# Performance work log

Hardware: AMD Instinct MI355X
Metric: run time of the kernel (lower is better)

The kernel has to match this reference:

```python
import jax, jax.numpy as jnp
import numpy as np

NUM_NODES, MEM_DIM, MSG_DIM, TIME_DIM = 65536, 128, 128, 128
POS_DIM = MEM_DIM  # PositionMessage reshape forces pos_embedding_dim == memory_dim
IN_MEM = MSG_DIM + 2 * MEM_DIM + TIME_DIM  # IdentityMessage width = 512
IN_POS = POS_DIM + 2 * MEM_DIM + TIME_DIM  # PositionMessage width = 512


def setup_inputs() -> dict:
    key = jax.random.key(0)
    ks = jax.random.split(key, 24)
    s = jnp.float32(0.05)
    f = lambda k, sh: jax.random.normal(k, sh, jnp.float32)
    return dict(
        n_id=jnp.arange(NUM_NODES, dtype=jnp.int32),
        memory=f(ks[0], (NUM_NODES, MEM_DIM)),
        pos_mem=f(ks[1], (NUM_NODES, MEM_DIM)),
        pos_emb=f(ks[2], (NUM_NODES, POS_DIM)),
        raw_msg_s=f(ks[3], (NUM_NODES, MSG_DIM)),
        raw_msg_d=f(ks[4], (NUM_NODES, MSG_DIM)),
        other_s=jax.random.randint(ks[5], (NUM_NODES,), 0, NUM_NODES, jnp.int32),
        other_d=jax.random.randint(ks[6], (NUM_NODES,), 0, NUM_NODES, jnp.int32),
        t_s=jax.random.randint(ks[7], (NUM_NODES,), 1000, 2000, jnp.int32),
        t_d=jax.random.randint(ks[8], (NUM_NODES,), 1000, 2000, jnp.int32),
        last_update=jax.random.randint(ks[9], (NUM_NODES,), 0, 1000, jnp.int32),
        w_time_mem=f(ks[10], (TIME_DIM,)) * s, b_time_mem=f(ks[11], (TIME_DIM,)) * s,
        w_time_pos=f(ks[12], (TIME_DIM,)) * s, b_time_pos=f(ks[13], (TIME_DIM,)) * s,
        Wih_mem=f(ks[14], (3 * MEM_DIM, IN_MEM)) * s, Whh_mem=f(ks[15], (3 * MEM_DIM, MEM_DIM)) * s,
        bih_mem=f(ks[16], (3 * MEM_DIM,)) * s, bhh_mem=f(ks[17], (3 * MEM_DIM,)) * s,
        Wih_pos=f(ks[18], (3 * MEM_DIM, IN_POS)) * s, Whh_pos=f(ks[19], (3 * MEM_DIM, MEM_DIM)) * s,
        bih_pos=f(ks[20], (3 * MEM_DIM,)) * s, bhh_pos=f(ks[21], (3 * MEM_DIM,)) * s,
    )


def _time_enc(t_rel, w, b):
    # PyG TimeEncoder: cos(Linear(1, time_dim)(t_rel))
    return jnp.cos(t_rel[:, None] * w[None, :] + b[None, :])


def _gru(x, h, Wih, Whh, bih, bhh):
    # torch.nn.GRUCell math
    gi = x @ Wih.T + bih
    gh = h @ Whh.T + bhh
    ir, iz, inn = jnp.split(gi, 3, axis=-1)
    hr, hz, hn = jnp.split(gh, 3, axis=-1)
    r = jax.nn.sigmoid(ir + hr)
    z = jax.nn.sigmoid(iz + hz)
    n = jnp.tanh(inn + r * hn)
    return (1.0 - z) * n + z * h


def _tgn_memory(mem, n_id, other_s, other_d, feat_s, feat_d, t_s, t_d,
                last_update, w_t, b_t, Wih, Whh, bih, bhh):
    # Gather per-node state; each node owns one src-store and one dst-store message.
    h = mem[n_id]                                        # [N, D]
    lu = last_update[n_id].astype(jnp.float32)
    te_s = _time_enc(t_s.astype(jnp.float32) - lu, w_t, b_t)
    te_d = _time_enc(t_d.astype(jnp.float32) - lu, w_t, b_t)
    msg_s = jnp.concatenate([h, mem[other_s], feat_s, te_s], axis=-1)  # [N, IN]
    msg_d = jnp.concatenate([h, mem[other_d], feat_d, te_d], axis=-1)
    # LastAggregator: keep the most recent message per node (scatter_max on t)
    pick_s = (t_s >= t_d)[:, None]
    aggr = jnp.where(pick_s, msg_s, msg_d)
    z = _gru(aggr, h, Wih, Whh, bih, bhh)
    new_lu = jnp.maximum(t_s, t_d)
    return z, new_lu


def reference(n_id, memory, pos_mem, pos_emb, raw_msg_s, raw_msg_d,
              other_s, other_d, t_s, t_d, last_update,
              w_time_mem, b_time_mem, w_time_pos, b_time_pos,
              Wih_mem, Whh_mem, bih_mem, bhh_mem,
              Wih_pos, Whh_pos, bih_pos, bhh_pos):
    z, last_up = _tgn_memory(memory, n_id, other_s, other_d, raw_msg_s, raw_msg_d,
                             t_s, t_d, last_update,
                             w_time_mem, b_time_mem, Wih_mem, Whh_mem, bih_mem, bhh_mem)
    # pos raw message is the event's src node id -> embedding lookup
    pos_z, _ = _tgn_memory(pos_mem, n_id, other_s, other_d,
                           pos_emb[n_id], pos_emb[other_d],
                           t_s, t_d, last_update,
                           w_time_pos, b_time_pos, Wih_pos, Whh_pos, bih_pos, bhh_pos)
    return z, pos_z, last_up
```

## Files before the change

kernel.cpp:

```cpp
#include <hip/hip_runtime.h>
#include <hip/hip_bf16.h>
#include <math.h>

#define NODES   65536
#define DD      128
#define BM      64
#define NSUB    24
#define WTILE_STRIDE (NSUB * 64 * 8)
#define WG_STRIDE    (20 * WTILE_STRIDE)

typedef __bf16 bf16x8 __attribute__((ext_vector_type(8)));
typedef float  f32x4  __attribute__((ext_vector_type(4)));

static __device__ __forceinline__ unsigned short f2bf(float f) {
    union { float f; unsigned u; } v; v.f = f;
    return (unsigned short)((v.u + 0x8000u) >> 16);
}
static __device__ __forceinline__ ushort4 pack4(float4 v) {
    ushort4 p;
    p.x = f2bf(v.x); p.y = f2bf(v.y); p.z = f2bf(v.z); p.w = f2bf(v.w);
    return p;
}
static __device__ __forceinline__ float fastcos(float x) {
    float r = x * 0.15915494309189535f;
    r = r - floorf(r);
    return __builtin_amdgcn_cosf(r);
}
static __device__ __forceinline__ float fsigmoid(float x) {
    return 1.0f / (1.0f + __expf(-x));
}
static __device__ __forceinline__ float ftanh(float x) {
    float ax = fabsf(x);
    float t  = __expf(-2.0f * ax);
    float th = 1.0f - 2.0f * t / (1.0f + t);
    return copysignf(th, x);
}

__global__ void prep_w_kernel(const float* __restrict__ Wih0, const float* __restrict__ Whh0,
                              const float* __restrict__ Wih1, const float* __restrict__ Whh1,
                              unsigned short* __restrict__ Wws) {
    int gid = blockIdx.x * 256 + threadIdx.x;
    if (gid >= 2 * WG_STRIDE) return;
    int g   = gid / WG_STRIDE;
    int r   = gid - g * WG_STRIDE;
    int kt  = r / WTILE_STRIDE;
    int r2  = r - kt * WTILE_STRIDE;
    int t   = r2 >> 9;
    int l8  = r2 & 511;
    int lane = l8 >> 3, j = l8 & 7;
    int cl  = lane & 15, q = lane >> 4;
    int n   = t * 16 + cl;
    const float* Wih = g ? Wih1 : Wih0;
    const float* Whh = g ? Whh1 : Whh0;
    float v;
    if (kt < 16) v = Wih[n * 512 + kt * 32 + q * 8 + j];
    else         v = Whh[n * 128 + (kt - 16) * 32 + q * 8 + j];
    Wws[gid] = f2bf(v);
}


#define KTILE(st)                                                              \
    do {                                                                       \
        bf16x8 a[4];                                                           \
        _Pragma("unroll")                                                      \
        for (int j = 0; j < 4; ++j)                                            \
            a[j] = *(const bf16x8*)(Xb + (j * 16 + cl) * 1024 +                \
                                    (((st) * 64 + q * 16) ^ swz));             \
        const unsigned short* wk = wbase + (size_t)(st) * WTILE_STRIDE;        \
        bf16x8 bR = *(const bf16x8*)(wk + tR * 512);                           \
        bf16x8 bZ = *(const bf16x8*)(wk + tZ * 512);                           \
        bf16x8 bN = *(const bf16x8*)(wk + tN * 512);                           \
        _Pragma("unroll")                                                      \
        for (int j = 0; j < 4; ++j) {                                          \
            acc[j * 4 + 0] = __builtin_amdgcn_mfma_f32_16x16x32_bf16(a[j], bR, acc[j * 4 + 0], 0, 0, 0); \
            acc[j * 4 + 1] = __builtin_amdgcn_mfma_f32_16x16x32_bf16(a[j], bZ, acc[j * 4 + 1], 0, 0, 0); \
            acc[j * 4 + 2] = __builtin_amdgcn_mfma_f32_16x16x32_bf16(a[j], bN, acc[j * 4 + 2], 0, 0, 0); \
        }                                                                      \
    } while (0)

#define KTILE2(st)                                                             \
    do {                                                                       \
        bf16x8 a[4];                                                           \
        _Pragma("unroll")                                                      \
        for (int j = 0; j < 4; ++j)                                            \
            a[j] = *(const bf16x8*)(Xb + (j * 16 + cl) * 1024 +                \
                                    (((st) * 64 + q * 16) ^ swz));             \
        const unsigned short* wk = wbase + (size_t)(st) * WTILE_STRIDE;        \
        const unsigned short* wh = wbase + (size_t)(16 + (st)) * WTILE_STRIDE; \
        bf16x8 bR = *(const bf16x8*)(wk + tR * 512);                           \
        bf16x8 bZ = *(const bf16x8*)(wk + tZ * 512);                           \
        bf16x8 bN = *(const bf16x8*)(wk + tN * 512);                           \
        bf16x8 cR = *(const bf16x8*)(wh + tR * 512);                           \
        bf16x8 cZ = *(const bf16x8*)(wh + tZ * 512);                           \
        bf16x8 cN = *(const bf16x8*)(wh + tN * 512);                           \
        _Pragma("unroll")                                                      \
        for (int j = 0; j < 4; ++j) {                                          \
            acc[j * 4 + 0] = __builtin_amdgcn_mfma_f32_16x16x32_bf16(a[j], bR, acc[j * 4 + 0], 0, 0, 0); \
            acc[j * 4 + 1] = __builtin_amdgcn_mfma_f32_16x16x32_bf16(a[j], bZ, acc[j * 4 + 1], 0, 0, 0); \
            acc[j * 4 + 2] = __builtin_amdgcn_mfma_f32_16x16x32_bf16(a[j], bN, acc[j * 4 + 2], 0, 0, 0); \
            acc[j * 4 + 0] = __builtin_amdgcn_mfma_f32_16x16x32_bf16(a[j], cR, acc[j * 4 + 0], 0, 0, 0); \
            acc[j * 4 + 1] = __builtin_amdgcn_mfma_f32_16x16x32_bf16(a[j], cZ, acc[j * 4 + 1], 0, 0, 0); \
            acc[j * 4 + 3] = __builtin_amdgcn_mfma_f32_16x16x32_bf16(a[j], cN, acc[j * 4 + 3], 0, 0, 0); \
        }                                                                      \
    } while (0)

__global__ __launch_bounds__(512, 4) void tgn_fused_kernel(
    const int*   __restrict__ n_id,
    const float* __restrict__ memory_,
    const float* __restrict__ pos_mem,
    const float* __restrict__ pos_emb,
    const float* __restrict__ raw_s,
    const float* __restrict__ raw_d,
    const int*   __restrict__ other_s,
    const int*   __restrict__ other_d,
    const int*   __restrict__ t_s,
    const int*   __restrict__ t_d,
    const int*   __restrict__ last_update,
    const float* __restrict__ w_time_mem, const float* __restrict__ b_time_mem,
    const float* __restrict__ w_time_pos, const float* __restrict__ b_time_pos,
    const float* __restrict__ bih_mem, const float* __restrict__ bhh_mem,
    const float* __restrict__ bih_pos, const float* __restrict__ bhh_pos,
    const unsigned short* __restrict__ Wws,
    float* __restrict__ out)
{
    __shared__ __align__(16) unsigned short X[BM * 512];
    __shared__ int   snid[BM];
    __shared__ int   soth[BM];
    __shared__ float sdt[BM];
    __shared__ int   sfeat[BM];

    const int g   = blockIdx.y;
    const int nb  = blockIdx.x;
    const int tid = threadIdx.x;
    const int lane = tid & 63;
    const int wv   = tid >> 6;

    const float* mem_g = g ? pos_mem    : memory_;
    const float* wt    = g ? w_time_pos : w_time_mem;
    const float* bt    = g ? b_time_pos : b_time_mem;
    const float* bih   = g ? bih_pos    : bih_mem;
    const float* bhh   = g ? bhh_pos    : bhh_mem;

    if (tid < BM) {
        int gi   = nb * BM + tid;
        int id   = n_id[gi];
        int ts   = t_s[gi];
        int td   = t_d[gi];
        bool pick = (ts >= td);
        int oth  = pick ? other_s[gi] : other_d[gi];
        int lu   = last_update[id];
        float dt = (float)(pick ? ts : td) - (float)lu;
        int code;
        if (g) code = pick ? id : other_d[gi];
        else   code = pick ? gi : ~gi;
        snid[tid]  = id;
        soth[tid]  = oth;
        sdt[tid]   = dt;
        sfeat[tid] = code;
        if (g == 0) {
            out[2 * (size_t)NODES * DD + gi] = (float)max(ts, td);
        }
    }
    __syncthreads();

    const int lc    = lane & 31;
    const int rh    = lane >> 5;
    const int srow0 = wv * 8;

    float4 wv4 = *(const float4*)(wt + lc * 4);
    float4 bv4 = *(const float4*)(bt + lc * 4);
    __builtin_amdgcn_sched_barrier(0);
    float4 hv[4];
    #pragma unroll
    for (int c = 0; c < 4; ++c) {
        int row = srow0 + 2 * c + rh;
        hv[c] = *(const float4*)(mem_g + (size_t)snid[row] * DD + lc * 4);
    }
    __builtin_amdgcn_sched_barrier(0);
    float4 of[4];
    #pragma unroll
    for (int c = 0; c < 4; ++c) {
        int row = srow0 + 2 * c + rh;
        of[c] = *(const float4*)(mem_g + (size_t)soth[row] * DD + lc * 4);
    }
    __builtin_amdgcn_sched_barrier(0);

    #pragma unroll
    for (int c = 0; c < 4; ++c) {
        int row = srow0 + 2 * c + rh;
        float dt = sdt[row];
        float4 tv;
        tv.x = fastcos(dt * wv4.x + bv4.x);
        tv.y = fastcos(dt * wv4.y + bv4.y);
        tv.z = fastcos(dt * wv4.z + bv4.z);
        tv.w = fastcos(dt * wv4.w + bv4.w);
        *(ushort4*)((char*)X + row * 1024 + ((768 + lc * 8) ^ ((row & 7) << 4))) = pack4(tv);
    }
    #pragma unroll
    for (int c = 0; c < 4; ++c) {
        int row = srow0 + 2 * c + rh;
        *(ushort4*)((char*)X + row * 1024 + ((lc * 8) ^ ((row & 7) << 4))) = pack4(hv[c]);
    }
    float4 ff[4];
    #pragma unroll
    for (int c = 0; c < 4; ++c) {
        int row = srow0 + 2 * c + rh;
        const float* src;
        if (g) {
            src = pos_emb + (size_t)sfeat[row] * DD;
        } else {
            int code = sfeat[row];
            src = code >= 0 ? raw_s + (size_t)code * DD
                            : raw_d + (size_t)(~code) * DD;
        }
        ff[c] = *(const float4*)(src + lc * 4);
    }
    __builtin_amdgcn_sched_barrier(0);
    #pragma unroll
    for (int c = 0; c < 4; ++c) {
        int row = srow0 + 2 * c + rh;
        *(ushort4*)((char*)X + row * 1024 + ((256 + lc * 8) ^ ((row & 7) << 4))) = pack4(of[c]);
    }
    #pragma unroll
    for (int c = 0; c < 4; ++c) {
        int row = srow0 + 2 * c + rh;
        *(ushort4*)((char*)X + row * 1024 + ((512 + lc * 8) ^ ((row & 7) << 4))) = pack4(ff[c]);
    }
    __syncthreads();

    f32x4 acc[16];
    #pragma unroll
    for (int i = 0; i < 16; ++i) acc[i] = (f32x4){0.f, 0.f, 0.f, 0.f};

    const int q  = lane >> 4;
    const int cl = lane & 15;
    const int swz = (cl & 7) << 4;
    const unsigned short* wbase = Wws + (size_t)g * WG_STRIDE + lane * 8;
    const int tR = wv, tZ = 8 + wv, tN = 16 + wv;
    const char* Xb = (const char*)X;

    __builtin_amdgcn_s_setprio(1);
    KTILE2(0); KTILE2(1); KTILE2(2); KTILE2(3);
    KTILE(4);  KTILE(5);  KTILE(6);  KTILE(7);
    KTILE(8);  KTILE(9);  KTILE(10); KTILE(11);
    KTILE(12); KTILE(13); KTILE(14); KTILE(15);
    __builtin_amdgcn_s_setprio(0);

    float* outz = out + (size_t)g * NODES * DD;
    const int d = wv * 16 + cl;
    float br  = bih[d]       + bhh[d];
    float bz  = bih[128 + d] + bhh[128 + d];
    float bni = bih[256 + d];
    float bnh = bhh[256 + d];
    #pragma unroll
    for (int j = 0; j < 4; ++j) {
        #pragma unroll
        for (int r = 0; r < 4; ++r) {
            int il = j * 16 + q * 4 + r;
            float rs  = acc[j * 4 + 0][r] + br;
            float zs  = acc[j * 4 + 1][r] + bz;
            float in_ = acc[j * 4 + 2][r] + bni;
            float hn_ = acc[j * 4 + 3][r] + bnh;
            float rg = fsigmoid(rs);
            float zg = fsigmoid(zs);
            float nv = ftanh(in_ + rg * hn_);
            float h  = mem_g[(size_t)snid[il] * DD + d];
            outz[(size_t)(nb * BM + il) * DD + d] = (1.0f - zg) * nv + zg * h;
        }
    }
}

extern "C" void kernel_launch(void* const* d_in, const int* in_sizes, int n_in,
                              void* d_out, int out_size, void* d_ws, size_t ws_size,
                              hipStream_t stream) {
    const int*   n_id        = (const int*)  d_in[0];
    const float* memory_     = (const float*)d_in[1];
    const float* pos_mem     = (const float*)d_in[2];
    const float* pos_emb     = (const float*)d_in[3];
    const float* raw_s       = (const float*)d_in[4];
    const float* raw_d       = (const float*)d_in[5];
    const int*   other_s     = (const int*)  d_in[6];
    const int*   other_d     = (const int*)  d_in[7];
    const int*   t_s         = (const int*)  d_in[8];
    const int*   t_d         = (const int*)  d_in[9];
    const int*   last_update = (const int*)  d_in[10];
    const float* w_time_mem  = (const float*)d_in[11];
    const float* b_time_mem  = (const float*)d_in[12];
    const float* w_time_pos  = (const float*)d_in[13];
    const float* b_time_pos  = (const float*)d_in[14];
    const float* Wih_mem     = (const float*)d_in[15];
    const float* Whh_mem     = (const float*)d_in[16];
    const float* bih_mem     = (const float*)d_in[17];
    const float* bhh_mem     = (const float*)d_in[18];
    const float* Wih_pos     = (const float*)d_in[19];
    const float* Whh_pos     = (const float*)d_in[20];
    const float* bih_pos     = (const float*)d_in[21];
    const float* bhh_pos     = (const float*)d_in[22];

    unsigned short* Wws = (unsigned short*)d_ws;
    float* out = (float*)d_out;

    prep_w_kernel<<<(2 * WG_STRIDE + 255) / 256, 256, 0, stream>>>(
        Wih_mem, Whh_mem, Wih_pos, Whh_pos, Wws);

    dim3 grid(NODES / BM, 2);
    tgn_fused_kernel<<<grid, 512, 0, stream>>>(
        n_id, memory_, pos_mem, pos_emb, raw_s, raw_d,
        other_s, other_d, t_s, t_d, last_update,
        w_time_mem, b_time_mem, w_time_pos, b_time_pos,
        bih_mem, bhh_mem, bih_pos, bhh_pos,
        Wws, out);
}
```

Measured before the change: 285.3 us.

## Fold Whh into Wih for r/z gates, rotate k-tiles, reuse LDS h

Precomputes Wih+Whh for the r and z gate columns that multiply h, since the first 128 input columns are h. This removes the separate hidden-state MFMAs for those gates, and only the n-gate hidden product is still computed separately. The k-loop start is rotated per block to spread weight and LDS accesses. The final interpolation reads h as bf16 from shared memory instead of fp32 from global memory, which saves a gather but lowers the precision of the h term.

```diff
diff --git a/kernel.cpp b/kernel.cpp
--- a/kernel.cpp
+++ b/kernel.cpp
@@ -5,6 +5,7 @@
 #define NODES   65536
 #define DD      128
 #define BM      64
+#define NST     16
 #define NSUB    24
 #define WTILE_STRIDE (NSUB * 64 * 8)
 #define WG_STRIDE    (20 * WTILE_STRIDE)
@@ -20,6 +21,10 @@
     ushort4 p;
     p.x = f2bf(v.x); p.y = f2bf(v.y); p.z = f2bf(v.z); p.w = f2bf(v.w);
     return p;
+}
+static __device__ __forceinline__ float bf2f(unsigned short u) {
+    union { unsigned u; float f; } v; v.u = ((unsigned)u) << 16;
+    return v.f;
 }
 static __device__ __forceinline__ float fastcos(float x) {
     float r = x * 0.15915494309189535f;
@@ -53,56 +58,15 @@
     const float* Wih = g ? Wih1 : Wih0;
     const float* Whh = g ? Whh1 : Whh0;
     float v;
-    if (kt < 16) v = Wih[n * 512 + kt * 32 + q * 8 + j];
-    else         v = Whh[n * 128 + (kt - 16) * 32 + q * 8 + j];
+    if (kt < 16) {
+        int k = kt * 32 + q * 8 + j;
+        v = Wih[n * 512 + k];
+        if (k < 128 && n < 256) v += Whh[n * 128 + k];
+    } else {
+        v = Whh[n * 128 + (kt - 16) * 32 + q * 8 + j];
+    }
     Wws[gid] = f2bf(v);
 }
-
-
-#define KTILE(st)                                                              \
-    do {                                                                       \
-        bf16x8 a[4];                                                           \
-        _Pragma("unroll")                                                      \
-        for (int j = 0; j < 4; ++j)                                            \
-            a[j] = *(const bf16x8*)(Xb + (j * 16 + cl) * 1024 +                \
-                                    (((st) * 64 + q * 16) ^ swz));             \
-        const unsigned short* wk = wbase + (size_t)(st) * WTILE_STRIDE;        \
-        bf16x8 bR = *(const bf16x8*)(wk + tR * 512);                           \
-        bf16x8 bZ = *(const bf16x8*)(wk + tZ * 512);                           \
-        bf16x8 bN = *(const bf16x8*)(wk + tN * 512);                           \
-        _Pragma("unroll")                                                      \
-        for (int j = 0; j < 4; ++j) {                                          \
-            acc[j * 4 + 0] = __builtin_amdgcn_mfma_f32_16x16x32_bf16(a[j], bR, acc[j * 4 + 0], 0, 0, 0); \
-            acc[j * 4 + 1] = __builtin_amdgcn_mfma_f32_16x16x32_bf16(a[j], bZ, acc[j * 4 + 1], 0, 0, 0); \
-            acc[j * 4 + 2] = __builtin_amdgcn_mfma_f32_16x16x32_bf16(a[j], bN, acc[j * 4 + 2], 0, 0, 0); \
-        }                                                                      \
-    } while (0)
-
-#define KTILE2(st)                                                             \
-    do {                                                                       \
-        bf16x8 a[4];                                                           \
-        _Pragma("unroll")                                                      \
-        for (int j = 0; j < 4; ++j)                                            \
-            a[j] = *(const bf16x8*)(Xb + (j * 16 + cl) * 1024 +                \
-                                    (((st) * 64 + q * 16) ^ swz));             \
-        const unsigned short* wk = wbase + (size_t)(st) * WTILE_STRIDE;        \
-        const unsigned short* wh = wbase + (size_t)(16 + (st)) * WTILE_STRIDE; \
-        bf16x8 bR = *(const bf16x8*)(wk + tR * 512);                           \
-        bf16x8 bZ = *(const bf16x8*)(wk + tZ * 512);                           \
-        bf16x8 bN = *(const bf16x8*)(wk + tN * 512);                           \
-        bf16x8 cR = *(const bf16x8*)(wh + tR * 512);                           \
-        bf16x8 cZ = *(const bf16x8*)(wh + tZ * 512);                           \
-        bf16x8 cN = *(const bf16x8*)(wh + tN * 512);                           \
-        _Pragma("unroll")                                                      \
-        for (int j = 0; j < 4; ++j) {                                          \
-            acc[j * 4 + 0] = __builtin_amdgcn_mfma_f32_16x16x32_bf16(a[j], bR, acc[j * 4 + 0], 0, 0, 0); \
-            acc[j * 4 + 1] = __builtin_amdgcn_mfma_f32_16x16x32_bf16(a[j], bZ, acc[j * 4 + 1], 0, 0, 0); \
-            acc[j * 4 + 2] = __builtin_amdgcn_mfma_f32_16x16x32_bf16(a[j], bN, acc[j * 4 + 2], 0, 0, 0); \
-            acc[j * 4 + 0] = __builtin_amdgcn_mfma_f32_16x16x32_bf16(a[j], cR, acc[j * 4 + 0], 0, 0, 0); \
-            acc[j * 4 + 1] = __builtin_amdgcn_mfma_f32_16x16x32_bf16(a[j], cZ, acc[j * 4 + 1], 0, 0, 0); \
-            acc[j * 4 + 3] = __builtin_amdgcn_mfma_f32_16x16x32_bf16(a[j], cN, acc[j * 4 + 3], 0, 0, 0); \
-        }                                                                      \
-    } while (0)
 
 __global__ __launch_bounds__(512, 4) void tgn_fused_kernel(
     const int*   __restrict__ n_id,
@@ -239,11 +203,34 @@
     const int tR = wv, tZ = 8 + wv, tN = 16 + wv;
     const char* Xb = (const char*)X;
 
+    const int r0 = (nb & 3) * 4;
+
     __builtin_amdgcn_s_setprio(1);
-    KTILE2(0); KTILE2(1); KTILE2(2); KTILE2(3);
-    KTILE(4);  KTILE(5);  KTILE(6);  KTILE(7);
-    KTILE(8);  KTILE(9);  KTILE(10); KTILE(11);
-    KTILE(12); KTILE(13); KTILE(14); KTILE(15);
+    #pragma unroll
+    for (int i = 0; i < NST; ++i) {
+        const int st = (i + r0) & 15;
+        bf16x8 a[4];
+        #pragma unroll
+        for (int j = 0; j < 4; ++j)
+            a[j] = *(const bf16x8*)(Xb + (j * 16 + cl) * 1024 + ((st * 64 + q * 16) ^ swz));
+        const unsigned short* wk = wbase + (size_t)st * WTILE_STRIDE;
+        bf16x8 bR = *(const bf16x8*)(wk + tR * 512);
+        bf16x8 bZ = *(const bf16x8*)(wk + tZ * 512);
+        bf16x8 bN = *(const bf16x8*)(wk + tN * 512);
+        #pragma unroll
+        for (int j = 0; j < 4; ++j) {
+            acc[j * 4 + 0] = __builtin_amdgcn_mfma_f32_16x16x32_bf16(a[j], bR, acc[j * 4 + 0], 0, 0, 0);
+            acc[j * 4 + 1] = __builtin_amdgcn_mfma_f32_16x16x32_bf16(a[j], bZ, acc[j * 4 + 1], 0, 0, 0);
+            acc[j * 4 + 2] = __builtin_amdgcn_mfma_f32_16x16x32_bf16(a[j], bN, acc[j * 4 + 2], 0, 0, 0);
+        }
+        if (st < 4) {
+            const unsigned short* wh = wbase + (size_t)(16 + st) * WTILE_STRIDE;
+            bf16x8 cN = *(const bf16x8*)(wh + tN * 512);
+            #pragma unroll
+            for (int j = 0; j < 4; ++j)
+                acc[j * 4 + 3] = __builtin_amdgcn_mfma_f32_16x16x32_bf16(a[j], cN, acc[j * 4 + 3], 0, 0, 0);
+        }
+    }
     __builtin_amdgcn_s_setprio(0);
 
     float* outz = out + (size_t)g * NODES * DD;
@@ -264,7 +251,7 @@
             float rg = fsigmoid(rs);
             float zg = fsigmoid(zs);
             float nv = ftanh(in_ + rg * hn_);
-            float h  = mem_g[(size_t)snid[il] * DD + d];
+            float h  = bf2f(*(const unsigned short*)(Xb + il * 1024 + ((2 * d) ^ ((il & 7) << 4))));
             outz[(size_t)(nb * BM + il) * DD + d] = (1.0f - zg) * nv + zg * h;
         }
     }
```

New measurement: 287.8 us. No clear change (+0.9%).
